# Kernel optimization log

Hardware: AMD Instinct MI355X
Metric: run time of the kernel (lower is better)

## Reference

```python
import jax, jax.numpy as jnp
import numpy as np

N, E, CLIP, HID, H, P, MD, B = 4096, 16384, 512, 1024, 4, 4, 512, 32
OUT2 = P * MD  # 2048


def prelu(x, a):
    return jnp.where(x >= 0, x, a * x)


def add_self_loops(src, dst, edge_attr, n):
    # PyG fill_value='mean': self-loop edge_attr = mean of incoming edge attrs
    sums = jax.ops.segment_sum(edge_attr, dst, num_segments=n)
    cnt = jax.ops.segment_sum(jnp.ones((dst.shape[0], 1), edge_attr.dtype), dst, num_segments=n)
    loop_attr = sums / jnp.maximum(cnt, 1.0)
    idx = jnp.arange(n)
    return (jnp.concatenate([src, idx]), jnp.concatenate([dst, idx]),
            jnp.concatenate([edge_attr, loop_attr], axis=0))


def gat_conv(x, src, dst, edge_attr, W, asrc, adst, We, ae, bias, heads, c):
    # PyG GATConv, concat=False (mean over heads), edge_dim used only in attention
    n = x.shape[0]
    src, dst, edge_attr = add_self_loops(src, dst, edge_attr, n)
    h = (x @ W).reshape(n, heads, c)                      # [N,H,C]
    e = (edge_attr @ We).reshape(-1, heads, c)            # [E',H,C]
    a_s = jnp.einsum('nhc,hc->nh', h, asrc)
    a_d = jnp.einsum('nhc,hc->nh', h, adst)
    a_e = jnp.einsum('ehc,hc->eh', e, ae)
    alpha = jax.nn.leaky_relu(a_s[src] + a_d[dst] + a_e, 0.2)  # [E',H]
    amax = jax.ops.segment_max(alpha, dst, num_segments=n)
    ex = jnp.exp(alpha - amax[dst])
    denom = jax.ops.segment_sum(ex, dst, num_segments=n)
    w = ex / jnp.maximum(denom[dst], 1e-16)
    msg = h[src] * w[:, :, None]                          # [E',H,C]
    out = jax.ops.segment_sum(msg, dst, num_segments=n)   # [N,H,C]
    return out.mean(axis=1) + bias


def attentional_pool(x, batch, gW1, gb1, gp1, gW2, gb2, gp2, gW3, gb3, n_graphs):
    gate = prelu(x @ gW1 + gb1, gp1)
    gate = prelu(gate @ gW2 + gb2, gp2)
    gate = gate @ gW3 + gb3                               # [N,1]
    gmax = jax.ops.segment_max(gate, batch, num_segments=n_graphs)
    ex = jnp.exp(gate - gmax[batch])
    denom = jax.ops.segment_sum(ex, batch, num_segments=n_graphs)
    s = ex / jnp.maximum(denom[batch], 1e-16)             # [N,1]
    return jax.ops.segment_sum(s * x, batch, num_segments=n_graphs)  # [B,F]


def setup_inputs() -> dict:
    key = jax.random.key(0)
    ks = jax.random.split(key, 24)
    sc = 0.05
    inp = {
        'x': jax.random.normal(ks[0], (N, CLIP), jnp.float32),
        'edge_index': jax.random.randint(ks[1], (2, E), 0, N),
        'edge_attr': jax.random.normal(ks[2], (E, CLIP), jnp.float32),
        'batch': jnp.sort(jax.random.randint(ks[3], (N,), 0, B)),
        # GATConv 1
        'W1': jax.random.normal(ks[4], (CLIP, H * HID), jnp.float32) * sc,
        'asrc1': jax.random.normal(ks[5], (H, HID), jnp.float32) * sc,
        'adst1': jax.random.normal(ks[6], (H, HID), jnp.float32) * sc,
        'We1': jax.random.normal(ks[7], (CLIP, H * HID), jnp.float32) * sc,
        'ae1': jax.random.normal(ks[8], (H, HID), jnp.float32) * sc,
        'b1': jnp.zeros((HID,), jnp.float32),
        'p1': jnp.float32(0.25),
        # GATConv 2
        'W2': jax.random.normal(ks[9], (HID, H * OUT2), jnp.float32) * sc,
        'asrc2': jax.random.normal(ks[10], (H, OUT2), jnp.float32) * sc,
        'adst2': jax.random.normal(ks[11], (H, OUT2), jnp.float32) * sc,
        'We2': jax.random.normal(ks[12], (CLIP, H * OUT2), jnp.float32) * sc,
        'ae2': jax.random.normal(ks[13], (H, OUT2), jnp.float32) * sc,
        'b2': jnp.zeros((OUT2,), jnp.float32),
        'p2': jnp.float32(0.25),
        # AttentionalAggregation gate_nn
        'gW1': jax.random.normal(ks[14], (OUT2, HID), jnp.float32) * sc,
        'gb1': jnp.zeros((HID,), jnp.float32),
        'gp1': jnp.float32(0.25),
        'gW2': jax.random.normal(ks[15], (HID, HID), jnp.float32) * sc,
        'gb2': jnp.zeros((HID,), jnp.float32),
        'gp2': jnp.float32(0.25),
        'gW3': jax.random.normal(ks[16], (HID, 1), jnp.float32) * sc,
        'gb3': jnp.zeros((1,), jnp.float32),
    }
    return inp


def reference(x, edge_index, edge_attr, batch,
              W1, asrc1, adst1, We1, ae1, b1, p1,
              W2, asrc2, adst2, We2, ae2, b2, p2,
              gW1, gb1, gp1, gW2, gb2, gp2, gW3, gb3):
    src, dst = edge_index[0], edge_index[1]
    h = gat_conv(x, src, dst, edge_attr, W1, asrc1, adst1, We1, ae1, b1, H, HID)
    h = prelu(h, p1)
    h = gat_conv(h, src, dst, edge_attr, W2, asrc2, adst2, We2, ae2, b2, H, OUT2)
    h = prelu(h, p2)
    pooled = attentional_pool(h, batch, gW1, gb1, gp1, gW2, gb2, gp2, gW3, gb3, B)
    return pooled.reshape(-1, P, MD)  # [B, prefix_length, mbart_dim]
```

## Files before the change

kernel.cpp:

```cpp
#include <hip/hip_runtime.h>
#include <hip/hip_bf16.h>
#include <math.h>

#define N_NODES 4096
#define N_EDGES 16384
#define CLIPD   512
#define HID     1024
#define NH      4
#define OUTD    2048
#define NB      32

typedef __bf16 bf16_t;
typedef bf16_t bf16x8 __attribute__((ext_vector_type(8)));
typedef float f32x4 __attribute__((ext_vector_type(4)));
typedef unsigned short u16x8 __attribute__((ext_vector_type(8)));

static __device__ __forceinline__ float lrelu(float x) { return x >= 0.f ? x : 0.2f * x; }

static __device__ __forceinline__ unsigned short f2bf(float f) {
  union { float f; unsigned int u; } v; v.f = f;
  unsigned int u = v.u;
  unsigned int r = (u + 0x7FFFu + ((u >> 16) & 1u)) >> 16;
  return (unsigned short)r;
}
static __device__ __forceinline__ float bf2f(unsigned short u) {
  union { unsigned int i; float f; } v; v.i = ((unsigned int)u) << 16; return v.f;
}

#define GLDS(g, l) __builtin_amdgcn_global_load_lds( \
    (const __attribute__((address_space(1))) void*)(g), \
    (__attribute__((address_space(3))) void*)(l), 16, 0, 0)

__device__ __forceinline__ void stcvt_tile(float (*t)[33], const float* __restrict__ in,
                                           unsigned short* __restrict__ out,
                                           int K1, int N1, int NHH, int h, int bx, int by,
                                           float scale) {
  const int k0 = by * 32, n0 = bx * 32;
  const int tx = threadIdx.x & 31, ty = threadIdx.x >> 5;
#pragma unroll
  for (int i = 0; i < 4; ++i)
    t[ty + 8 * i][tx] = in[(size_t)(k0 + ty + 8 * i) * (NHH * N1) + (size_t)h * N1 + n0 + tx];
  __syncthreads();
#pragma unroll
  for (int i = 0; i < 4; ++i)
    out[(size_t)(n0 + ty + 8 * i) * (NHH * K1) + (size_t)h * K1 + k0 + tx] =
        f2bf(scale * t[tx][ty + 8 * i]);
}

__device__ __forceinline__ void vfold(float (*r1)[NH], float (*r2)[NH],
                                      const float* __restrict__ W,
                                      const float* __restrict__ a1v, const float* __restrict__ a2v,
                                      float* __restrict__ o1, float* __restrict__ o2, int C, int k) {
  const int tid = threadIdx.x;
  const float* row = W + (size_t)k * (NH * C);
  float x1[NH] = {0.f, 0.f, 0.f, 0.f}, x2[NH] = {0.f, 0.f, 0.f, 0.f};
  for (int c = tid; c < C; c += 256) {
    for (int h = 0; h < NH; ++h) {
      float w = row[h * C + c];
      x1[h] += w * a1v[h * C + c];
      x2[h] += w * a2v[h * C + c];
    }
  }
  for (int h = 0; h < NH; ++h)
    for (int o = 32; o > 0; o >>= 1) {
      x1[h] += __shfl_down(x1[h], o);
      x2[h] += __shfl_down(x2[h], o);
    }
  const int wid = tid >> 6, lane = tid & 63;
  if (lane == 0)
    for (int h = 0; h < NH; ++h) { r1[wid][h] = x1[h]; r2[wid][h] = x2[h]; }
  __syncthreads();
  if (tid < NH)
    o1[k * NH + tid] = r1[0][tid] + r1[1][tid] + r1[2][tid] + r1[3][tid];
  else if (o2 != nullptr && tid < 2 * NH) {
    int h = tid - NH;
    o2[k * NH + h] = r2[0][h] + r2[1][h] + r2[2][h] + r2[3][h];
  }
}

__global__ __launch_bounds__(256) void prep_kernel(
    const float* __restrict__ W1, const float* __restrict__ W2,
    const float* __restrict__ gW1, const float* __restrict__ gW2,
    unsigned short* __restrict__ B1t, unsigned short* __restrict__ B2t,
    unsigned short* __restrict__ gW1t, unsigned short* __restrict__ gW2t,
    const float* __restrict__ We1, const float* __restrict__ ae1w,
    const float* __restrict__ We2, const float* __restrict__ ae2w,
    const float* __restrict__ asrc1, const float* __restrict__ adst1,
    const float* __restrict__ asrc2, const float* __restrict__ adst2,
    float* __restrict__ v1, float* __restrict__ v2,
    float* __restrict__ us1, float* __restrict__ ud1,
    float* __restrict__ us2, float* __restrict__ ud2) {
  __shared__ float t[32][33];
  __shared__ float r1[4][NH], r2[4][NH];
  const int id = blockIdx.x;
  if (id < 2048) {
    int h = id >> 9, r = id & 511;
    stcvt_tile(t, W1, B1t, CLIPD, HID, NH, h, r & 31, r >> 5, 0.25f);
  } else if (id < 10240) {
    int r2_ = id - 2048;
    int h = r2_ >> 11, r = r2_ & 2047;
    stcvt_tile(t, W2, B2t, HID, OUTD, NH, h, r & 63, r >> 6, 0.25f);
  } else if (id < 12288) {
    int r = id - 10240;
    stcvt_tile(t, gW1, gW1t, OUTD, HID, 1, 0, r & 31, r >> 5, 1.0f);
  } else if (id < 13312) {
    int r = id - 12288;
    stcvt_tile(t, gW2, gW2t, HID, HID, 1, 0, r & 31, r >> 5, 1.0f);
  } else {
    int vid = id - 13312;
    if (vid < 512)       vfold(r1, r2, We1, ae1w, ae1w, v1, nullptr, HID, vid);
    else if (vid < 1024) vfold(r1, r2, We2, ae2w, ae2w, v2, nullptr, OUTD, vid - 512);
    else if (vid < 1536) vfold(r1, r2, W1, asrc1, adst1, us1, ud1, HID, vid - 1024);
    else                 vfold(r1, r2, W2, asrc2, adst2, us2, ud2, OUTD, vid - 1536);
  }
}

__global__ __launch_bounds__(1024) void csr_kernel(const int* __restrict__ ei,
                                                   int* __restrict__ offs,
                                                   int* __restrict__ csr_src, int* __restrict__ csr_eid) {
  __shared__ int sdeg[N_NODES];
  __shared__ int soffs[N_NODES];
  __shared__ int sscan[1024];
  const int t = threadIdx.x;
  for (int i = t; i < N_NODES; i += 1024) sdeg[i] = 0;
  __syncthreads();
  for (int e = t; e < N_EDGES; e += 1024) atomicAdd(&sdeg[ei[N_EDGES + e]], 1);
  __syncthreads();
  const int d0 = sdeg[4 * t], d1 = sdeg[4 * t + 1], d2 = sdeg[4 * t + 2], d3 = sdeg[4 * t + 3];
  sscan[t] = d0 + d1 + d2 + d3;
  __syncthreads();
  for (int off = 1; off < 1024; off <<= 1) {
    int v = (t >= off) ? sscan[t - off] : 0;
    __syncthreads();
    sscan[t] += v;
    __syncthreads();
  }
  const int base = (t > 0) ? sscan[t - 1] : 0;
  soffs[4 * t] = base;
  soffs[4 * t + 1] = base + d0;
  soffs[4 * t + 2] = base + d0 + d1;
  soffs[4 * t + 3] = base + d0 + d1 + d2;
#pragma unroll
  for (int j = 0; j < 4; ++j) offs[4 * t + j] = soffs[4 * t + j];
  if (t == 1023) offs[N_NODES] = sscan[1023];
  sdeg[4 * t] = 0; sdeg[4 * t + 1] = 0; sdeg[4 * t + 2] = 0; sdeg[4 * t + 3] = 0;
  __syncthreads();
  for (int e = t; e < N_EDGES; e += 1024) {
    int dst = ei[N_EDGES + e];
    int pos = soffs[dst] + atomicAdd(&sdeg[dst], 1);
    csr_src[pos] = ei[e];
    csr_eid[pos] = e;
  }
}

__global__ __launch_bounds__(256) void aexprep_kernel(
    const float* __restrict__ ea, const int* __restrict__ ei,
    const float* __restrict__ v1, const float* __restrict__ v2,
    float* __restrict__ ae1, float* __restrict__ ae2,
    float* __restrict__ aesum1, float* __restrict__ aesum2,
    const float* __restrict__ x, const float* __restrict__ us, const float* __restrict__ ud,
    unsigned short* __restrict__ xb, float* __restrict__ as_, float* __restrict__ ad_) {
  __shared__ float4 s0[CLIPD];
  __shared__ float4 s1[CLIPD];
  const int tid = threadIdx.x;
  const int wid = tid >> 6, lane = tid & 63;
  if (blockIdx.x < 256) {
    s0[tid] = ((const float4*)v1)[tid];
    s0[tid + 256] = ((const float4*)v1)[tid + 256];
    s1[tid] = ((const float4*)v2)[tid];
    s1[tid + 256] = ((const float4*)v2)[tid + 256];
    __syncthreads();
    for (int i = 0; i < 16; ++i) {
      const int e = blockIdx.x * 64 + wid * 16 + i;
      const float* row = ea + (size_t)e * CLIPD;
      float a1[NH] = {0.f, 0.f, 0.f, 0.f}, a2[NH] = {0.f, 0.f, 0.f, 0.f};
      for (int k = lane; k < CLIPD; k += 64) {
        float xv = row[k];
        float4 w1 = s0[k];
        float4 w2 = s1[k];
        a1[0] += xv * w1.x; a1[1] += xv * w1.y; a1[2] += xv * w1.z; a1[3] += xv * w1.w;
        a2[0] += xv * w2.x; a2[1] += xv * w2.y; a2[2] += xv * w2.z; a2[3] += xv * w2.w;
      }
      for (int h = 0; h < NH; ++h)
        for (int o = 32; o > 0; o >>= 1) {
          a1[h] += __shfl_down(a1[h], o);
          a2[h] += __shfl_down(a2[h], o);
        }
      if (lane == 0) {
        int dst = ei[N_EDGES + e];
        for (int h = 0; h < NH; ++h) {
          ae1[e * NH + h] = a1[h];
          ae2[e * NH + h] = a2[h];
          atomicAdd(&aesum1[dst * NH + h], a1[h]);
          atomicAdd(&aesum2[dst * NH + h], a2[h]);
        }
      }
    }
  } else {
    for (int k = tid; k < CLIPD; k += 256) {
      s0[k] = ((const float4*)us)[k];
      s1[k] = ((const float4*)ud)[k];
    }
    __syncthreads();
    const int n = (blockIdx.x - 256) * 4 + wid;
    const float* row = x + (size_t)n * CLIPD;
    unsigned short* orow = xb + (size_t)n * CLIPD;
    float s[NH] = {0.f, 0.f, 0.f, 0.f}, d[NH] = {0.f, 0.f, 0.f, 0.f};
    for (int q = lane; q < CLIPD / 4; q += 64) {
      float4 xv = ((const float4*)row)[q];
      ushort4 ob;
      ob.x = f2bf(xv.x); ob.y = f2bf(xv.y); ob.z = f2bf(xv.z); ob.w = f2bf(xv.w);
      ((ushort4*)orow)[q] = ob;
      const float* xp = &xv.x;
#pragma unroll
      for (int j = 0; j < 4; ++j) {
        float xs = xp[j];
        float4 u = s0[q * 4 + j], v = s1[q * 4 + j];
        s[0] += xs * u.x; s[1] += xs * u.y; s[2] += xs * u.z; s[3] += xs * u.w;
        d[0] += xs * v.x; d[1] += xs * v.y; d[2] += xs * v.z; d[3] += xs * v.w;
      }
    }
#pragma unroll
    for (int h = 0; h < NH; ++h)
      for (int o = 32; o > 0; o >>= 1) {
        s[h] += __shfl_down(s[h], o);
        d[h] += __shfl_down(d[h], o);
      }
    if (lane == 0)
      for (int h = 0; h < NH; ++h) {
        as_[n * NH + h] = s[h];
        ad_[n * NH + h] = d[h];
      }
  }
}

__global__ __launch_bounds__(256) void rowdot_o(const unsigned short* __restrict__ rows,
                                                const float* __restrict__ us, const float* __restrict__ ud,
                                                float* __restrict__ as_, float* __restrict__ ad_) {
  __shared__ float4 su[HID], sd[HID];
  const int tid = threadIdx.x;
  for (int k = tid; k < HID; k += 256) {
    su[k] = ((const float4*)us)[k];
    sd[k] = ((const float4*)ud)[k];
  }
  __syncthreads();
  const int wid = tid >> 6, lane = tid & 63;
  const int n = blockIdx.x * 4 + wid;
  const unsigned short* row = rows + (size_t)n * HID;
  float s[NH] = {0.f, 0.f, 0.f, 0.f}, d[NH] = {0.f, 0.f, 0.f, 0.f};
  for (int k2 = lane; k2 < HID / 2; k2 += 64) {
    ushort2 uv = ((const ushort2*)row)[k2];
    float f0 = bf2f(uv.x), f1 = bf2f(uv.y);
    float4 u0 = su[2 * k2], u1 = su[2 * k2 + 1];
    float4 v0 = sd[2 * k2], v1 = sd[2 * k2 + 1];
    s[0] += f0 * u0.x + f1 * u1.x; s[1] += f0 * u0.y + f1 * u1.y;
    s[2] += f0 * u0.z + f1 * u1.z; s[3] += f0 * u0.w + f1 * u1.w;
    d[0] += f0 * v0.x + f1 * v1.x; d[1] += f0 * v0.y + f1 * v1.y;
    d[2] += f0 * v0.z + f1 * v1.z; d[3] += f0 * v0.w + f1 * v1.w;
  }
#pragma unroll
  for (int h = 0; h < NH; ++h)
    for (int o = 32; o > 0; o >>= 1) {
      s[h] += __shfl_down(s[h], o);
      d[h] += __shfl_down(d[h], o);
    }
  if (lane == 0)
    for (int h = 0; h < NH; ++h) {
      as_[n * NH + h] = s[h];
      ad_[n * NH + h] = d[h];
    }
}

template<int C>
__global__ __launch_bounds__(256) void aggw_kernel(const unsigned short* __restrict__ src,
                                                   const float* __restrict__ as_, const float* __restrict__ ad_,
                                                   const float* __restrict__ aee, const float* __restrict__ aesum,
                                                   const int* __restrict__ offs, const int* __restrict__ csr_src,
                                                   const int* __restrict__ csr_eid,
                                                   unsigned short* __restrict__ out) {
  constexpr int CPT = C / 64;
  const int lane = threadIdx.x & 63;
  const int n = blockIdx.x * 4 + (threadIdx.x >> 6);
  const int off = offs[n];
  const int deg = offs[n + 1] - off;
  const int h = lane >> 4, slot = lane & 15;
  const float4 ad4 = *(const float4*)&ad_[n * NH];
  const float4 as4 = *(const float4*)&as_[n * NH];
  const float4 ae4 = *(const float4*)&aesum[n * NH];
  const float adn = ((const float*)&ad4)[h];
  const float aself = lrelu(((const float*)&as4)[h] + adn +
                            ((const float*)&ae4)[h] / fmaxf((float)deg, 1.f));
  float m = (slot == 0) ? aself : -3.0e38f;
  for (int i = slot; i < deg; i += 16) {
    float a = lrelu(as_[csr_src[off + i] * NH + h] + adn + aee[csr_eid[off + i] * NH + h]);
    m = fmaxf(m, a);
  }
#pragma unroll
  for (int o = 1; o < 16; o <<= 1) m = fmaxf(m, __shfl_xor(m, o));
  float den = (slot == 0) ? __expf(aself - m) : 0.f;
  for (int i = slot; i < deg; i += 16) {
    float a = lrelu(as_[csr_src[off + i] * NH + h] + adn + aee[csr_eid[off + i] * NH + h]);
    den += __expf(a - m);
  }
#pragma unroll
  for (int o = 1; o < 16; o <<= 1) den += __shfl_xor(den, o);
  const float wself_l = __expf(aself - m) / den;
  float mh[NH], dh[NH], wsh[NH];
#pragma unroll
  for (int hh = 0; hh < NH; ++hh) {
    mh[hh] = __shfl(m, hh * 16);
    dh[hh] = 1.0f / __shfl(den, hh * 16);
    wsh[hh] = __shfl(wself_l, hh * 16);
  }
  float acc[NH][CPT];
#pragma unroll
  for (int hh = 0; hh < NH; ++hh)
#pragma unroll
    for (int c = 0; c < CPT; ++c) acc[hh][c] = 0.f;
  for (int i = 0; i < deg; ++i) {
    const int sidx = csr_src[off + i];
    const float4 asv = *(const float4*)&as_[sidx * NH];
    const float4 aev = *(const float4*)&aee[csr_eid[off + i] * NH];
    float w[NH];
#pragma unroll
    for (int hh = 0; hh < NH; ++hh)
      w[hh] = __expf(lrelu(((const float*)&asv)[hh] + ((const float*)&ad4)[hh] +
                           ((const float*)&aev)[hh]) - mh[hh]) * dh[hh];
    const unsigned short* hp = src + (size_t)sidx * C + lane * CPT;
#pragma unroll
    for (int v8 = 0; v8 < CPT / 8; ++v8) {
      u16x8 u = *(const u16x8*)(hp + v8 * 8);
#pragma unroll
      for (int c = 0; c < 8; ++c) {
        float f = bf2f(u[c]);
#pragma unroll
        for (int hh = 0; hh < NH; ++hh) acc[hh][v8 * 8 + c] += w[hh] * f;
      }
    }
  }
  {
    const unsigned short* hp = src + (size_t)n * C + lane * CPT;
#pragma unroll
    for (int v8 = 0; v8 < CPT / 8; ++v8) {
      u16x8 u = *(const u16x8*)(hp + v8 * 8);
#pragma unroll
      for (int c = 0; c < 8; ++c) {
        float f = bf2f(u[c]);
#pragma unroll
        for (int hh = 0; hh < NH; ++hh) acc[hh][v8 * 8 + c] += wsh[hh] * f;
      }
    }
  }
#pragma unroll
  for (int hh = 0; hh < NH; ++hh) {
#pragma unroll
    for (int v8 = 0; v8 < CPT / 8; ++v8) {
      u16x8 o;
#pragma unroll
      for (int c = 0; c < 8; ++c) o[c] = f2bf(acc[hh][v8 * 8 + c]);
      *(u16x8*)&out[((size_t)n * NH + hh) * C + lane * CPT + v8 * 8] = o;
    }
  }
}

template<int EPI, int WF, int BN, int GATE>
__global__ __launch_bounds__(256) void mfma_gemm(const unsigned short* __restrict__ A,
                                                 const unsigned short* __restrict__ Bt,
                                                 unsigned short* __restrict__ C,
                                                 float* __restrict__ Cf,
                                                 int M, int N, int K,
                                                 const float* __restrict__ bias,
                                                 const float* __restrict__ pa,
                                                 const float* __restrict__ g3,
                                                 float* __restrict__ gate) {
  constexpr int NFR = BN / 32;
  __shared__ unsigned short As[128 * 32];
  __shared__ unsigned short Bs[BN * 32];
  const int nwg = gridDim.x * gridDim.y;
  int id = blockIdx.y * gridDim.x + blockIdx.x;
  id = (id & 7) * (nwg >> 3) + (id >> 3);
  const int bx = id % gridDim.x, by = id / gridDim.x;
  const int tid = threadIdx.x;
  const int lane = tid & 63;
  const int w = tid >> 6;
  const int wr = w >> 1, wc = w & 1;
  const int brow = by * 128, bcol = bx * BN;
  const int r0 = tid >> 2;
  const int koff = (tid & 3) * 8;
  const int fr = lane & 15;
  const int fk = (lane >> 4) * 8;
  f32x4 acc[4][NFR] = {};
  for (int kt = 0; kt < K; kt += 32) {
    GLDS(A + (size_t)(brow + r0) * K + kt + koff, &As[tid * 8]);
    GLDS(A + (size_t)(brow + 64 + r0) * K + kt + koff, &As[2048 + tid * 8]);
    GLDS(Bt + (size_t)(bcol + r0) * K + kt + koff, &Bs[tid * 8]);
    if constexpr (BN == 128)
      GLDS(Bt + (size_t)(bcol + 64 + r0) * K + kt + koff, &Bs[2048 + tid * 8]);
    asm volatile("s_waitcnt vmcnt(0)" ::: "memory");
    __syncthreads();
    bf16x8 af[4], bfr[NFR];
#pragma unroll
    for (int mi = 0; mi < 4; ++mi)
      af[mi] = *(const bf16x8*)&As[(wr * 64 + mi * 16 + fr) * 32 + fk];
#pragma unroll
    for (int ni = 0; ni < NFR; ++ni)
      bfr[ni] = *(const bf16x8*)&Bs[(wc * (BN / 2) + ni * 16 + fr) * 32 + fk];
#pragma unroll
    for (int mi = 0; mi < 4; ++mi)
#pragma unroll
      for (int ni = 0; ni < NFR; ++ni)
        acc[mi][ni] = __builtin_amdgcn_mfma_f32_16x16x32_bf16(af[mi], bfr[ni], acc[mi][ni], 0, 0, 0);
    __syncthreads();
  }
  const float ap = EPI ? *pa : 0.f;
  float g3v[NFR];
  if constexpr (GATE) {
#pragma unroll
    for (int ni = 0; ni < NFR; ++ni) g3v[ni] = g3[bcol + wc * (BN / 2) + ni * 16 + fr];
  }
#pragma unroll
  for (int mi = 0; mi < 4; ++mi) {
    const int rb = brow + wr * 64 + mi * 16 + (lane >> 4) * 4;
    if constexpr (GATE) {
#pragma unroll
      for (int r = 0; r < 4; ++r) {
        float p = 0.f;
#pragma unroll
        for (int ni = 0; ni < NFR; ++ni) {
          const int col = bcol + wc * (BN / 2) + ni * 16 + fr;
          float v = acc[mi][ni][r] + bias[col];
          v = v >= 0.f ? v : ap * v;
          p += v * g3v[ni];
        }
#pragma unroll
        for (int o = 1; o < 16; o <<= 1) p += __shfl_xor(p, o);
        if (fr == 0) atomicAdd(&gate[rb + r], p);
      }
    } else {
#pragma unroll
      for (int ni = 0; ni < NFR; ++ni) {
        const int col = bcol + wc * (BN / 2) + ni * 16 + fr;
        float bv = 0.f;
        if (EPI) bv = bias[col];
#pragma unroll
        for (int r = 0; r < 4; ++r) {
          float v = acc[mi][ni][r];
          if (EPI) { v += bv; v = v >= 0.f ? v : ap * v; }
          C[(size_t)(rb + r) * N + col] = f2bf(v);
          if (WF) Cf[(size_t)(rb + r) * N + col] = v;
        }
      }
    }
  }
}

__global__ __launch_bounds__(256) void pool2_kernel(const float* __restrict__ out2,
                                                    const float* __restrict__ gate,
                                                    const int* __restrict__ batch,
                                                    float* __restrict__ dout) {
  const int b = blockIdx.y;
  const int tid = threadIdx.x;
  const int col = blockIdx.x * 256 + tid;
  int lo = 0, hi = N_NODES;
  while (lo < hi) { int mid = (lo + hi) >> 1; if (batch[mid] < b) lo = mid + 1; else hi = mid; }
  const int s = lo;
  hi = N_NODES;
  while (lo < hi) { int mid = (lo + hi) >> 1; if (batch[mid] < b + 1) lo = mid + 1; else hi = mid; }
  const int e = lo;
  __shared__ float red[4];
  const int wid = tid >> 6, lane = tid & 63;
  float m = -3.0e38f;
  for (int n = s + tid; n < e; n += 256) m = fmaxf(m, gate[n]);
  for (int o = 32; o > 0; o >>= 1) m = fmaxf(m, __shfl_down(m, o));
  if (lane == 0) red[wid] = m;
  __syncthreads();
  m = fmaxf(fmaxf(red[0], red[1]), fmaxf(red[2], red[3]));
  __syncthreads();
  float sum = 0.f;
  for (int n = s + tid; n < e; n += 256) sum += __expf(gate[n] - m);
  for (int o = 32; o > 0; o >>= 1) sum += __shfl_down(sum, o);
  if (lane == 0) red[wid] = sum;
  __syncthreads();
  sum = red[0] + red[1] + red[2] + red[3];
  const float gi = 1.0f / fmaxf(sum, 1e-16f);
  float acc = 0.f;
  for (int n = s; n < e; ++n)
    acc += __expf(gate[n] - m) * gi * out2[(size_t)n * OUTD + col];
  dout[(size_t)b * OUTD + col] = acc;
}

#define MB(x) ((size_t)(x) * 1048576)
#define WS_XB     MB(0)
#define WS_B1T    MB(4)
#define WS_B2T    MB(8)
#define WS_GW1T   MB(24)
#define WS_GW2T   MB(28)
#define WS_AGGX   MB(30)
#define WS_OUT1B  MB(46)
#define WS_AGGO   MB(54)
#define WS_OUT2F  MB(86)
#define WS_OUT2B  MB(118)
#define WS_GH1B   MB(134)
#define WS_SM     MB(142)
#define WS_AES1   (WS_SM + 0)
#define WS_AES2   (WS_AES1 + 65536)
#define WS_GATE   (WS_AES2 + 65536)
#define WS_ZBYTES 147456
#define WS_OFFS   (WS_GATE + 16384)
#define WS_CSRS   (WS_OFFS + 16640)
#define WS_CSRE   (WS_CSRS + 65536)
#define WS_AS1    (WS_CSRE + 65536)
#define WS_AD1    (WS_AS1 + 65536)
#define WS_AEE1   (WS_AD1 + 65536)
#define WS_AS2    (WS_AEE1 + 262144)
#define WS_AD2    (WS_AS2 + 65536)
#define WS_AEE2   (WS_AD2 + 65536)
#define WS_V1     (WS_AEE2 + 262144)
#define WS_V2     (WS_V1 + 8192)
#define WS_US1    (WS_V2 + 8192)
#define WS_UD1    (WS_US1 + 8192)
#define WS_US2    (WS_UD1 + 8192)
#define WS_UD2    (WS_US2 + 16384)

extern "C" void kernel_launch(void* const* d_in, const int* in_sizes, int n_in,
                              void* d_out, int out_size, void* d_ws, size_t ws_size,
                              hipStream_t stream) {
  const float* x     = (const float*)d_in[0];
  const int*   ei    = (const int*)d_in[1];
  const float* ea    = (const float*)d_in[2];
  const int*   batch = (const int*)d_in[3];
  const float* W1    = (const float*)d_in[4];
  const float* asrc1 = (const float*)d_in[5];
  const float* adst1 = (const float*)d_in[6];
  const float* We1   = (const float*)d_in[7];
  const float* ae1w  = (const float*)d_in[8];
  const float* b1    = (const float*)d_in[9];
  const float* p1    = (const float*)d_in[10];
  const float* W2    = (const float*)d_in[11];
  const float* asrc2 = (const float*)d_in[12];
  const float* adst2 = (const float*)d_in[13];
  const float* We2   = (const float*)d_in[14];
  const float* ae2w  = (const float*)d_in[15];
  const float* b2    = (const float*)d_in[16];
  const float* p2    = (const float*)d_in[17];
  const float* gW1   = (const float*)d_in[18];
  const float* gb1   = (const float*)d_in[19];
  const float* gp1   = (const float*)d_in[20];
  const float* gW2   = (const float*)d_in[21];
  const float* gb2   = (const float*)d_in[22];
  const float* gp2   = (const float*)d_in[23];
  const float* gW3   = (const float*)d_in[24];

  char* ws = (char*)d_ws;
  unsigned short* xb    = (unsigned short*)(ws + WS_XB);
  unsigned short* B1t   = (unsigned short*)(ws + WS_B1T);
  unsigned short* B2t   = (unsigned short*)(ws + WS_B2T);
  unsigned short* gW1t  = (unsigned short*)(ws + WS_GW1T);
  unsigned short* gW2t  = (unsigned short*)(ws + WS_GW2T);
  unsigned short* aggXb = (unsigned short*)(ws + WS_AGGX);
  unsigned short* out1b = (unsigned short*)(ws + WS_OUT1B);
  unsigned short* aggOb = (unsigned short*)(ws + WS_AGGO);
  float*          out2f = (float*)(ws + WS_OUT2F);
  unsigned short* out2b = (unsigned short*)(ws + WS_OUT2B);
  unsigned short* gh1b  = (unsigned short*)(ws + WS_GH1B);
  float* aesum1  = (float*)(ws + WS_AES1);
  float* aesum2  = (float*)(ws + WS_AES2);
  float* gate    = (float*)(ws + WS_GATE);
  int*   offs    = (int*)(ws + WS_OFFS);
  int*   csr_src = (int*)(ws + WS_CSRS);
  int*   csr_eid = (int*)(ws + WS_CSRE);
  float* as1     = (float*)(ws + WS_AS1);
  float* ad1     = (float*)(ws + WS_AD1);
  float* aee1    = (float*)(ws + WS_AEE1);
  float* as2     = (float*)(ws + WS_AS2);
  float* ad2     = (float*)(ws + WS_AD2);
  float* aee2    = (float*)(ws + WS_AEE2);
  float* v1      = (float*)(ws + WS_V1);
  float* v2      = (float*)(ws + WS_V2);
  float* us1     = (float*)(ws + WS_US1);
  float* ud1     = (float*)(ws + WS_UD1);
  float* us2     = (float*)(ws + WS_US2);
  float* ud2     = (float*)(ws + WS_UD2);
  float* dout    = (float*)d_out;

  hipMemsetAsync(ws + WS_AES1, 0, WS_ZBYTES, stream);

  csr_kernel<<<1, 1024, 0, stream>>>(ei, offs, csr_src, csr_eid);
  prep_kernel<<<15872, 256, 0, stream>>>(W1, W2, gW1, gW2, B1t, B2t, gW1t, gW2t,
                                         We1, ae1w, We2, ae2w, asrc1, adst1, asrc2, adst2,
                                         v1, v2, us1, ud1, us2, ud2);
  aexprep_kernel<<<1280, 256, 0, stream>>>(ea, ei, v1, v2, aee1, aee2, aesum1, aesum2,
                                           x, us1, ud1, xb, as1, ad1);

  aggw_kernel<CLIPD><<<N_NODES / 4, 256, 0, stream>>>(xb, as1, ad1, aee1, aesum1,
                                                      offs, csr_src, csr_eid, aggXb);
  mfma_gemm<1, 0, 64, 0><<<dim3(HID / 64, N_NODES / 128), 256, 0, stream>>>(
      aggXb, B1t, out1b, nullptr, N_NODES, HID, NH * CLIPD, b1, p1, nullptr, nullptr);

  rowdot_o<<<N_NODES / 4, 256, 0, stream>>>(out1b, us2, ud2, as2, ad2);
  aggw_kernel<HID><<<N_NODES / 4, 256, 0, stream>>>(out1b, as2, ad2, aee2, aesum2,
                                                    offs, csr_src, csr_eid, aggOb);
  mfma_gemm<1, 1, 64, 0><<<dim3(OUTD / 64, N_NODES / 128), 256, 0, stream>>>(
      aggOb, B2t, out2b, out2f, N_NODES, OUTD, NH * HID, b2, p2, nullptr, nullptr);

  mfma_gemm<1, 0, 64, 0><<<dim3(HID / 64, N_NODES / 128), 256, 0, stream>>>(
      out2b, gW1t, gh1b, nullptr, N_NODES, HID, OUTD, gb1, gp1, nullptr, nullptr);
  mfma_gemm<1, 0, 64, 1><<<dim3(HID / 64, N_NODES / 128), 256, 0, stream>>>(
      gh1b, gW2t, nullptr, nullptr, N_NODES, HID, HID, gb2, gp2, gW3, gate);

  pool2_kernel<<<dim3(OUTD / 256, NB), 256, 0, stream>>>(out2f, gate, batch, dout);
}
```

Before: 587.0 us.

## Fuse CSR build into prep kernel and rowdot into layer-1 GEMM epilogue

The single-block CSR construction moves into block 0 of the prep kernel, using a 256-thread wave-shuffle scan, so it runs alongside the weight conversion instead of as a separate serial launch. The rowdot_o kernel is removed and its per-node attention dot products are computed in the first GEMM's epilogue and accumulated with atomics into zeroed buffers. The edge-attention prep is split over more blocks, and the second GAT GEMM uses a 128-wide N tile. The fused epilogue adds per-column loads, shuffles and atomics, and computes on fp32 values rather than the rounded bf16 output, which slightly changes the numerics.

```diff
diff --git a/kernel.cpp b/kernel.cpp
--- a/kernel.cpp
+++ b/kernel.cpp
@@ -78,6 +78,50 @@
   }
 }
 
+__device__ __forceinline__ void csr_path(const int* __restrict__ ei, int* __restrict__ offs,
+                                         int* __restrict__ csr_src, int* __restrict__ csr_eid,
+                                         char* smem) {
+  int* sdeg  = (int*)smem;
+  int* soffs = (int*)(smem + 16384);
+  int* swsum = (int*)(smem + 32768);
+  const int t = threadIdx.x;
+  for (int i = t; i < N_NODES; i += 256) sdeg[i] = 0;
+  __syncthreads();
+  for (int e = t; e < N_EDGES; e += 256) atomicAdd(&sdeg[ei[N_EDGES + e]], 1);
+  __syncthreads();
+  int loc[16];
+  int mysum = 0;
+#pragma unroll
+  for (int j = 0; j < 16; ++j) { loc[j] = sdeg[t * 16 + j]; mysum += loc[j]; }
+  const int lane = t & 63, wid = t >> 6;
+  int incl = mysum;
+  for (int o = 1; o < 64; o <<= 1) {
+    int v = __shfl_up(incl, o);
+    if (lane >= o) incl += v;
+  }
+  if (lane == 63) swsum[wid] = incl;
+  __syncthreads();
+  int wbase = 0;
+  for (int w = 0; w < wid; ++w) wbase += swsum[w];
+  int run = wbase + incl - mysum;
+#pragma unroll
+  for (int j = 0; j < 16; ++j) {
+    soffs[t * 16 + j] = run;
+    offs[t * 16 + j] = run;
+    run += loc[j];
+  }
+  if (t == 255) offs[N_NODES] = run;
+  __syncthreads();
+  for (int i = t; i < N_NODES; i += 256) sdeg[i] = 0;
+  __syncthreads();
+  for (int e = t; e < N_EDGES; e += 256) {
+    int dst = ei[N_EDGES + e];
+    int pos = soffs[dst] + atomicAdd(&sdeg[dst], 1);
+    csr_src[pos] = ei[e];
+    csr_eid[pos] = e;
+  }
+}
+
 __global__ __launch_bounds__(256) void prep_kernel(
     const float* __restrict__ W1, const float* __restrict__ W2,
     const float* __restrict__ gW1, const float* __restrict__ gW2,
@@ -89,67 +133,36 @@
     const float* __restrict__ asrc2, const float* __restrict__ adst2,
     float* __restrict__ v1, float* __restrict__ v2,
     float* __restrict__ us1, float* __restrict__ ud1,
-    float* __restrict__ us2, float* __restrict__ ud2) {
-  __shared__ float t[32][33];
-  __shared__ float r1[4][NH], r2[4][NH];
+    float* __restrict__ us2, float* __restrict__ ud2,
+    const int* __restrict__ ei, int* __restrict__ offs,
+    int* __restrict__ csr_src, int* __restrict__ csr_eid) {
+  __shared__ __align__(16) char smem[33040];
+  float (*t)[33]  = (float(*)[33])smem;
+  float (*r1)[NH] = (float(*)[NH])(smem + 4224);
+  float (*r2)[NH] = (float(*)[NH])(smem + 4288);
   const int id = blockIdx.x;
-  if (id < 2048) {
-    int h = id >> 9, r = id & 511;
+  if (id == 0) {
+    csr_path(ei, offs, csr_src, csr_eid, smem);
+  } else if (id <= 2048) {
+    int r = id - 1;
+    int h = r >> 9; r &= 511;
     stcvt_tile(t, W1, B1t, CLIPD, HID, NH, h, r & 31, r >> 5, 0.25f);
-  } else if (id < 10240) {
-    int r2_ = id - 2048;
-    int h = r2_ >> 11, r = r2_ & 2047;
+  } else if (id <= 10240) {
+    int r = id - 2049;
+    int h = r >> 11; r &= 2047;
     stcvt_tile(t, W2, B2t, HID, OUTD, NH, h, r & 63, r >> 6, 0.25f);
-  } else if (id < 12288) {
-    int r = id - 10240;
+  } else if (id <= 12288) {
+    int r = id - 10241;
     stcvt_tile(t, gW1, gW1t, OUTD, HID, 1, 0, r & 31, r >> 5, 1.0f);
-  } else if (id < 13312) {
-    int r = id - 12288;
+  } else if (id <= 13312) {
+    int r = id - 12289;
     stcvt_tile(t, gW2, gW2t, HID, HID, 1, 0, r & 31, r >> 5, 1.0f);
   } else {
-    int vid = id - 13312;
+    int vid = id - 13313;
     if (vid < 512)       vfold(r1, r2, We1, ae1w, ae1w, v1, nullptr, HID, vid);
     else if (vid < 1024) vfold(r1, r2, We2, ae2w, ae2w, v2, nullptr, OUTD, vid - 512);
     else if (vid < 1536) vfold(r1, r2, W1, asrc1, adst1, us1, ud1, HID, vid - 1024);
     else                 vfold(r1, r2, W2, asrc2, adst2, us2, ud2, OUTD, vid - 1536);
-  }
-}
-
-__global__ __launch_bounds__(1024) void csr_kernel(const int* __restrict__ ei,
-                                                   int* __restrict__ offs,
-                                                   int* __restrict__ csr_src, int* __restrict__ csr_eid) {
-  __shared__ int sdeg[N_NODES];
-  __shared__ int soffs[N_NODES];
-  __shared__ int sscan[1024];
-  const int t = threadIdx.x;
-  for (int i = t; i < N_NODES; i += 1024) sdeg[i] = 0;
-  __syncthreads();
-  for (int e = t; e < N_EDGES; e += 1024) atomicAdd(&sdeg[ei[N_EDGES + e]], 1);
-  __syncthreads();
-  const int d0 = sdeg[4 * t], d1 = sdeg[4 * t + 1], d2 = sdeg[4 * t + 2], d3 = sdeg[4 * t + 3];
-  sscan[t] = d0 + d1 + d2 + d3;
-  __syncthreads();
-  for (int off = 1; off < 1024; off <<= 1) {
-    int v = (t >= off) ? sscan[t - off] : 0;
-    __syncthreads();
-    sscan[t] += v;
-    __syncthreads();
-  }
-  const int base = (t > 0) ? sscan[t - 1] : 0;
-  soffs[4 * t] = base;
-  soffs[4 * t + 1] = base + d0;
-  soffs[4 * t + 2] = base + d0 + d1;
-  soffs[4 * t + 3] = base + d0 + d1 + d2;
-#pragma unroll
-  for (int j = 0; j < 4; ++j) offs[4 * t + j] = soffs[4 * t + j];
-  if (t == 1023) offs[N_NODES] = sscan[1023];
-  sdeg[4 * t] = 0; sdeg[4 * t + 1] = 0; sdeg[4 * t + 2] = 0; sdeg[4 * t + 3] = 0;
-  __syncthreads();
-  for (int e = t; e < N_EDGES; e += 1024) {
-    int dst = ei[N_EDGES + e];
-    int pos = soffs[dst] + atomicAdd(&sdeg[dst], 1);
-    csr_src[pos] = ei[e];
-    csr_eid[pos] = e;
   }
 }
 
@@ -164,14 +177,14 @@
   __shared__ float4 s1[CLIPD];
   const int tid = threadIdx.x;
   const int wid = tid >> 6, lane = tid & 63;
-  if (blockIdx.x < 256) {
+  if (blockIdx.x < 512) {
     s0[tid] = ((const float4*)v1)[tid];
     s0[tid + 256] = ((const float4*)v1)[tid + 256];
     s1[tid] = ((const float4*)v2)[tid];
     s1[tid + 256] = ((const float4*)v2)[tid + 256];
     __syncthreads();
-    for (int i = 0; i < 16; ++i) {
-      const int e = blockIdx.x * 64 + wid * 16 + i;
+    for (int i = 0; i < 8; ++i) {
+      const int e = blockIdx.x * 32 + wid * 8 + i;
       const float* row = ea + (size_t)e * CLIPD;
       float a1[NH] = {0.f, 0.f, 0.f, 0.f}, a2[NH] = {0.f, 0.f, 0.f, 0.f};
       for (int k = lane; k < CLIPD; k += 64) {
@@ -202,7 +215,7 @@
       s1[k] = ((const float4*)ud)[k];
     }
     __syncthreads();
-    const int n = (blockIdx.x - 256) * 4 + wid;
+    const int n = (blockIdx.x - 512) * 4 + wid;
     const float* row = x + (size_t)n * CLIPD;
     unsigned short* orow = xb + (size_t)n * CLIPD;
     float s[NH] = {0.f, 0.f, 0.f, 0.f}, d[NH] = {0.f, 0.f, 0.f, 0.f};
@@ -232,43 +245,6 @@
         ad_[n * NH + h] = d[h];
       }
   }
-}
-
-__global__ __launch_bounds__(256) void rowdot_o(const unsigned short* __restrict__ rows,
-                                                const float* __restrict__ us, const float* __restrict__ ud,
-                                                float* __restrict__ as_, float* __restrict__ ad_) {
-  __shared__ float4 su[HID], sd[HID];
-  const int tid = threadIdx.x;
-  for (int k = tid; k < HID; k += 256) {
-    su[k] = ((const float4*)us)[k];
-    sd[k] = ((const float4*)ud)[k];
-  }
-  __syncthreads();
-  const int wid = tid >> 6, lane = tid & 63;
-  const int n = blockIdx.x * 4 + wid;
-  const unsigned short* row = rows + (size_t)n * HID;
-  float s[NH] = {0.f, 0.f, 0.f, 0.f}, d[NH] = {0.f, 0.f, 0.f, 0.f};
-  for (int k2 = lane; k2 < HID / 2; k2 += 64) {
-    ushort2 uv = ((const ushort2*)row)[k2];
-    float f0 = bf2f(uv.x), f1 = bf2f(uv.y);
-    float4 u0 = su[2 * k2], u1 = su[2 * k2 + 1];
-    float4 v0 = sd[2 * k2], v1 = sd[2 * k2 + 1];
-    s[0] += f0 * u0.x + f1 * u1.x; s[1] += f0 * u0.y + f1 * u1.y;
-    s[2] += f0 * u0.z + f1 * u1.z; s[3] += f0 * u0.w + f1 * u1.w;
-    d[0] += f0 * v0.x + f1 * v1.x; d[1] += f0 * v0.y + f1 * v1.y;
-    d[2] += f0 * v0.z + f1 * v1.z; d[3] += f0 * v0.w + f1 * v1.w;
-  }
-#pragma unroll
-  for (int h = 0; h < NH; ++h)
-    for (int o = 32; o > 0; o >>= 1) {
-      s[h] += __shfl_down(s[h], o);
-      d[h] += __shfl_down(d[h], o);
-    }
-  if (lane == 0)
-    for (int h = 0; h < NH; ++h) {
-      as_[n * NH + h] = s[h];
-      ad_[n * NH + h] = d[h];
-    }
 }
 
 template<int C>
@@ -363,7 +339,7 @@
   }
 }
 
-template<int EPI, int WF, int BN, int GATE>
+template<int EPI, int WF, int BN, int GATE, int RD>
 __global__ __launch_bounds__(256) void mfma_gemm(const unsigned short* __restrict__ A,
                                                  const unsigned short* __restrict__ Bt,
                                                  unsigned short* __restrict__ C,
@@ -372,7 +348,11 @@
                                                  const float* __restrict__ bias,
                                                  const float* __restrict__ pa,
                                                  const float* __restrict__ g3,
-                                                 float* __restrict__ gate) {
+                                                 float* __restrict__ gate,
+                                                 const float* __restrict__ rd_us,
+                                                 const float* __restrict__ rd_ud,
+                                                 float* __restrict__ rd_as,
+                                                 float* __restrict__ rd_ad) {
   constexpr int NFR = BN / 32;
   __shared__ unsigned short As[128 * 32];
   __shared__ unsigned short Bs[BN * 32];
@@ -436,6 +416,37 @@
         for (int o = 1; o < 16; o <<= 1) p += __shfl_xor(p, o);
         if (fr == 0) atomicAdd(&gate[rb + r], p);
       }
+    } else if constexpr (RD) {
+#pragma unroll
+      for (int r = 0; r < 4; ++r) {
+        float sa[NH] = {0.f, 0.f, 0.f, 0.f}, da[NH] = {0.f, 0.f, 0.f, 0.f};
+#pragma unroll
+        for (int ni = 0; ni < NFR; ++ni) {
+          const int col = bcol + wc * (BN / 2) + ni * 16 + fr;
+          float v = acc[mi][ni][r] + bias[col];
+          v = v >= 0.f ? v : ap * v;
+          C[(size_t)(rb + r) * N + col] = f2bf(v);
+          float4 u = ((const float4*)rd_us)[col];
+          float4 dd = ((const float4*)rd_ud)[col];
+          sa[0] += v * u.x; sa[1] += v * u.y; sa[2] += v * u.z; sa[3] += v * u.w;
+          da[0] += v * dd.x; da[1] += v * dd.y; da[2] += v * dd.z; da[3] += v * dd.w;
+        }
+#pragma unroll
+        for (int o = 1; o < 16; o <<= 1) {
+#pragma unroll
+          for (int hh = 0; hh < NH; ++hh) {
+            sa[hh] += __shfl_xor(sa[hh], o);
+            da[hh] += __shfl_xor(da[hh], o);
+          }
+        }
+        if (fr == 0) {
+#pragma unroll
+          for (int hh = 0; hh < NH; ++hh) {
+            atomicAdd(&rd_as[(rb + r) * NH + hh], sa[hh]);
+            atomicAdd(&rd_ad[(rb + r) * NH + hh], da[hh]);
+          }
+        }
+      }
     } else {
 #pragma unroll
       for (int ni = 0; ni < NFR; ++ni) {
@@ -505,16 +516,16 @@
 #define WS_AES1   (WS_SM + 0)
 #define WS_AES2   (WS_AES1 + 65536)
 #define WS_GATE   (WS_AES2 + 65536)
-#define WS_ZBYTES 147456
-#define WS_OFFS   (WS_GATE + 16384)
+#define WS_AS2    (WS_GATE + 16384)
+#define WS_AD2    (WS_AS2 + 65536)
+#define WS_ZBYTES 278528
+#define WS_OFFS   (WS_AD2 + 65536)
 #define WS_CSRS   (WS_OFFS + 16640)
 #define WS_CSRE   (WS_CSRS + 65536)
 #define WS_AS1    (WS_CSRE + 65536)
 #define WS_AD1    (WS_AS1 + 65536)
 #define WS_AEE1   (WS_AD1 + 65536)
-#define WS_AS2    (WS_AEE1 + 262144)
-#define WS_AD2    (WS_AS2 + 65536)
-#define WS_AEE2   (WS_AD2 + 65536)
+#define WS_AEE2   (WS_AEE1 + 262144)
 #define WS_V1     (WS_AEE2 + 262144)
 #define WS_V2     (WS_V1 + 8192)
 #define WS_US1    (WS_V2 + 8192)
@@ -566,14 +577,14 @@
   float* aesum1  = (float*)(ws + WS_AES1);
   float* aesum2  = (float*)(ws + WS_AES2);
   float* gate    = (float*)(ws + WS_GATE);
+  float* as2     = (float*)(ws + WS_AS2);
+  float* ad2     = (float*)(ws + WS_AD2);
   int*   offs    = (int*)(ws + WS_OFFS);
   int*   csr_src = (int*)(ws + WS_CSRS);
   int*   csr_eid = (int*)(ws + WS_CSRE);
   float* as1     = (float*)(ws + WS_AS1);
   float* ad1     = (float*)(ws + WS_AD1);
   float* aee1    = (float*)(ws + WS_AEE1);
-  float* as2     = (float*)(ws + WS_AS2);
-  float* ad2     = (float*)(ws + WS_AD2);
   float* aee2    = (float*)(ws + WS_AEE2);
   float* v1      = (float*)(ws + WS_V1);
   float* v2      = (float*)(ws + WS_V2);
@@ -585,28 +596,31 @@
 
   hipMemsetAsync(ws + WS_AES1, 0, WS_ZBYTES, stream);
 
-  csr_kernel<<<1, 1024, 0, stream>>>(ei, offs, csr_src, csr_eid);
-  prep_kernel<<<15872, 256, 0, stream>>>(W1, W2, gW1, gW2, B1t, B2t, gW1t, gW2t,
+  prep_kernel<<<15873, 256, 0, stream>>>(W1, W2, gW1, gW2, B1t, B2t, gW1t, gW2t,
                                          We1, ae1w, We2, ae2w, asrc1, adst1, asrc2, adst2,
-                                         v1, v2, us1, ud1, us2, ud2);
-  aexprep_kernel<<<1280, 256, 0, stream>>>(ea, ei, v1, v2, aee1, aee2, aesum1, aesum2,
+                                         v1, v2, us1, ud1, us2, ud2,
+                                         ei, offs, csr_src, csr_eid);
+  aexprep_kernel<<<1536, 256, 0, stream>>>(ea, ei, v1, v2, aee1, aee2, aesum1, aesum2,
                                            x, us1, ud1, xb, as1, ad1);
 
   aggw_kernel<CLIPD><<<N_NODES / 4, 256, 0, stream>>>(xb, as1, ad1, aee1, aesum1,
                                                       offs, csr_src, csr_eid, aggXb);
-  mfma_gemm<1, 0, 64, 0><<<dim3(HID / 64, N_NODES / 128), 256, 0, stream>>>(
-      aggXb, B1t, out1b, nullptr, N_NODES, HID, NH * CLIPD, b1, p1, nullptr, nullptr);
-
-  rowdot_o<<<N_NODES / 4, 256, 0, stream>>>(out1b, us2, ud2, as2, ad2);
+  mfma_gemm<1, 0, 64, 0, 1><<<dim3(HID / 64, N_NODES / 128), 256, 0, stream>>>(
+      aggXb, B1t, out1b, nullptr, N_NODES, HID, NH * CLIPD, b1, p1,
+      nullptr, nullptr, us2, ud2, as2, ad2);
+
   aggw_kernel<HID><<<N_NODES / 4, 256, 0, stream>>>(out1b, as2, ad2, aee2, aesum2,
                                                     offs, csr_src, csr_eid, aggOb);
-  mfma_gemm<1, 1, 64, 0><<<dim3(OUTD / 64, N_NODES / 128), 256, 0, stream>>>(
-      aggOb, B2t, out2b, out2f, N_NODES, OUTD, NH * HID, b2, p2, nullptr, nullptr);
-
-  mfma_gemm<1, 0, 64, 0><<<dim3(HID / 64, N_NODES / 128), 256, 0, stream>>>(
-      out2b, gW1t, gh1b, nullptr, N_NODES, HID, OUTD, gb1, gp1, nullptr, nullptr);
-  mfma_gemm<1, 0, 64, 1><<<dim3(HID / 64, N_NODES / 128), 256, 0, stream>>>(
-      gh1b, gW2t, nullptr, nullptr, N_NODES, HID, HID, gb2, gp2, gW3, gate);
+  mfma_gemm<1, 1, 128, 0, 0><<<dim3(OUTD / 128, N_NODES / 128), 256, 0, stream>>>(
+      aggOb, B2t, out2b, out2f, N_NODES, OUTD, NH * HID, b2, p2,
+      nullptr, nullptr, nullptr, nullptr, nullptr, nullptr);
+
+  mfma_gemm<1, 0, 64, 0, 0><<<dim3(HID / 64, N_NODES / 128), 256, 0, stream>>>(
+      out2b, gW1t, gh1b, nullptr, N_NODES, HID, OUTD, gb1, gp1,
+      nullptr, nullptr, nullptr, nullptr, nullptr, nullptr);
+  mfma_gemm<1, 0, 64, 1, 0><<<dim3(HID / 64, N_NODES / 128), 256, 0, stream>>>(
+      gh1b, gW2t, nullptr, nullptr, N_NODES, HID, HID, gb2, gp2,
+      gW3, gate, nullptr, nullptr, nullptr, nullptr);
 
   pool2_kernel<<<dim3(OUTD / 256, NB), 256, 0, stream>>>(out2f, gate, batch, dout);
 }
```

Result: slower. 623.2 us (+6.2%).
